# Performance work log

Measured on AMD Instinct MI355X. Metric: run time of the kernel, lower is better.

The kernel has to match this reference:

```python
import jax, jax.numpy as jnp
import numpy as np

STATIC_TH = 0.05
TRIM_RATIO = 0.2
EPS = 1e-6


def setup_inputs() -> dict:
    key = jax.random.key(0)
    k1, k2, k3 = jax.random.split(key, 3)
    B, T, H, W = 2, 32, 518, 518
    pred_disp = jax.random.uniform(k1, (B, T, H, W), jnp.float32, 0.01, 10.0)
    gt_depth = jax.random.uniform(k2, (B, T, H, W), jnp.float32, 0.1, 80.0)
    mask = jax.random.uniform(k3, (B, T, H, W)) > 0.2
    return {"pred_disp": pred_disp, "gt_depth": gt_depth, "mask": mask}


def _nanquantile_rows(vals, valid, q):
    """torch.nanquantile(dim=1, interpolation='linear') where invalid entries are NaN.
    vals: [N,Q] float, valid: [N,Q] bool. Returns [N] threshold (NaN if row empty)."""
    big = jnp.where(valid, vals, jnp.inf)          # invalid -> +inf, sorts to the end
    srt = jnp.sort(big, axis=1)                    # [N,Q]
    nv = valid.sum(axis=1)                         # valid count per row
    pos = q * jnp.maximum(nv - 1, 0).astype(vals.dtype)
    lo = jnp.floor(pos).astype(jnp.int32)
    hi = jnp.ceil(pos).astype(jnp.int32)
    frac = pos - lo.astype(vals.dtype)
    vlo = jnp.take_along_axis(srt, lo[:, None], axis=1)[:, 0]
    vhi = jnp.take_along_axis(srt, hi[:, None], axis=1)[:, 0]
    thresh = vlo * (1.0 - frac) + vhi * frac
    return jnp.where(nv > 0, thresh, jnp.nan)      # empty row -> NaN (keep-mask all False)


def reference(pred_disp, gt_depth, mask):
    B, T, H, W = pred_disp.shape
    raw = jnp.clip(pred_disp, EPS)                 # [B,T,H,W]
    gt_disp = 1.0 / jnp.clip(gt_depth, EPS)

    # per-batch least-squares scale/shift alignment on masked pixels
    raw_f = raw.reshape(B, -1)
    gt_f = gt_disp.reshape(B, -1)
    mf = mask.reshape(B, -1).astype(raw.dtype)
    count = jnp.maximum(mf.sum(axis=1, keepdims=True), 1.0)
    mean_raw = (raw_f * mf).sum(axis=1, keepdims=True) / count
    mean_gt = (gt_f * mf).sum(axis=1, keepdims=True) / count
    d_c = (raw_f - mean_raw) * mf
    g_c = (gt_f - mean_gt) * mf
    cov = (d_c * g_c).sum(axis=1, keepdims=True)
    var = jnp.maximum((d_c * d_c).sum(axis=1, keepdims=True), EPS)
    s = cov / var
    t = mean_gt - s * mean_raw
    aligned = (raw_f * s + t).reshape(B, T, H, W)

    # temporal gradient matching on static pixels
    d_diff = jnp.abs(aligned[:, 1:] - aligned[:, :-1])     # [B,T-1,H,W]
    g_diff = jnp.abs(gt_disp[:, 1:] - gt_disp[:, :-1])
    valid_pair = mask[:, 1:] & mask[:, :-1]
    depth_diff = jnp.abs(gt_depth[:, 1:] - gt_depth[:, :-1])
    static = valid_pair & (depth_diff < STATIC_TH)
    err = jnp.abs(d_diff - g_diff)

    N = B * (T - 1)
    Q = H * W
    err2 = err.reshape(N, Q)
    st2 = static.reshape(N, Q)

    # trimmed (robust) masked mean per frame pair
    thresh = _nanquantile_rows(err2, st2, 1.0 - TRIM_RATIO)   # [N]
    keep = st2 & (err2 <= thresh[:, None])
    sum_err = (err2 * keep.astype(err2.dtype)).sum(axis=1)
    cnt = jnp.maximum(keep.sum(axis=1).astype(err2.dtype), 1.0)
    loss_frame = sum_err / cnt
    return loss_frame.mean()
```

## Files before the change

kernel.cpp:

```cpp
#include <hip/hip_runtime.h>
#include <math.h>

#define HW      268324
#define HW4     67081
#define T_      32
#define B_      2
#define NPAIR   31
#define NROW    62
#define GX      263
#define CHUNKS  4
#define NBLKB   (CHUNKS*GX)
#define NFC     9
#define SLOTS   4
#define CAP     2048
#define CSTR    16
#define EPSF    1e-6f
#define STH     0.05f

typedef float fx4 __attribute__((ext_vector_type(4)));
typedef int   ix4 __attribute__((ext_vector_type(4)));


__device__ __forceinline__ float fast_rcp(float x) {
    float r = __builtin_amdgcn_rcpf(x);
    float e = fmaf(-x, r, 1.0f);
    return fmaf(r, e, r);
}

__device__ __forceinline__ fx4 nt_load4(const float* p) {
    return __builtin_nontemporal_load((const fx4*)p);
}
__device__ __forceinline__ ix4 nt_load4i(const int* p) {
    return __builtin_nontemporal_load((const ix4*)p);
}
__device__ __forceinline__ unsigned int nt_loadu(const unsigned char* p) {
    return __builtin_nontemporal_load((const unsigned int*)p);
}

template<int BYTEFMT>
__launch_bounds__(256)
__global__ void pass1_kernel(const float* __restrict__ pred,
                             const float* __restrict__ depth,
                             const void*  __restrict__ maskp,
                             double* __restrict__ partials,
                             int*    __restrict__ cnt,
                             float*  __restrict__ rbuf,
                             float*  __restrict__ gbuf,
                             float*  __restrict__ out)
{
    if (blockIdx.x == 0 && blockIdx.y == 0 && threadIdx.x == 0) out[0] = 0.0f;

    const int p4 = blockIdx.x * 256 + threadIdx.x;
    const bool active = (p4 < HW4);
    const int p4c = active ? p4 : (HW4 - 1);
    const int b = blockIdx.y >> 2;
    const int c = blockIdx.y & 3;
    const int fs = c * 8;
    const size_t base = (size_t)b * T_ * HW + (size_t)fs * HW + (size_t)p4c * 4;
    const size_t off8 = (size_t)((c == 3) ? 7 : 8) * HW;

    const float* pp = pred + base;
    const float* dd = depth + base;
    const unsigned char* m8 = (const unsigned char*)maskp + base;
    const int* m32 = (const int*)maskp + base;

    fx4 pvs[SLOTS], dvs[SLOTS];
    unsigned int mws[SLOTS];
    ix4 mis[SLOTS];

    #pragma unroll
    for (int k = 0; k < SLOTS - 1; ++k) {
        pvs[k] = nt_load4(pp + (size_t)k * HW);
        dvs[k] = nt_load4(dd + (size_t)k * HW);
        if (BYTEFMT) mws[k] = nt_loadu(m8 + (size_t)k * HW);
        else         mis[k] = nt_load4i(m32 + (size_t)k * HW);
    }

    int scn = 0;
    float f_r = 0.f, f_g = 0.f, f_rg = 0.f, f_rr = 0.f;
    float pcr[4], pcg[4], pcd[4];
    unsigned int pmb = 0u;

    #pragma unroll
    for (int k = 0; k < NFC; ++k) {
        const int kp = k + SLOTS - 1;
        if (kp < NFC) {
            const size_t off = (kp < 8) ? (size_t)kp * HW : off8;
            const int s2 = kp % SLOTS;
            pvs[s2] = nt_load4(pp + off);
            dvs[s2] = nt_load4(dd + off);
            if (BYTEFMT) mws[s2] = nt_loadu(m8 + off);
            else         mis[s2] = nt_load4i(m32 + off);
        }
        const int s = k % SLOTS;
        unsigned int mb;
        if (BYTEFMT) {
            const unsigned int w = mws[s];
            mb = ((w & 0x000000FFu) ? 1u : 0u) | ((w & 0x0000FF00u) ? 2u : 0u)
               | ((w & 0x00FF0000u) ? 4u : 0u) | ((w & 0xFF000000u) ? 8u : 0u);
        } else {
            const ix4 mi = mis[s];
            mb = (mi.x ? 1u : 0u) | (mi.y ? 2u : 0u) | (mi.z ? 4u : 0u) | (mi.w ? 8u : 0u);
        }
        if (!active) mb = 0u;

        const float px[4] = {pvs[s].x, pvs[s].y, pvs[s].z, pvs[s].w};
        const float dx[4] = {dvs[s].x, dvs[s].y, dvs[s].z, dvs[s].w};
        float cr[4], cg[4], cd[4];
        #pragma unroll
        for (int j = 0; j < 4; ++j) {
            cr[j] = fmaxf(px[j], EPSF);
            cd[j] = dx[j];
            cg[j] = fast_rcp(fmaxf(dx[j], EPSF));
        }

        if (k <= 7) {
            #pragma unroll
            for (int j = 0; j < 4; ++j) {
                const bool m = (mb >> j) & 1u;
                const float rm = m ? cr[j] : 0.0f;
                const float gm = m ? cg[j] : 0.0f;
                scn += m ? 1 : 0;
                f_r += rm; f_g += gm;
                f_rg = fmaf(rm, gm, f_rg);
                f_rr = fmaf(rm, rm, f_rr);
            }
        }

        if (k >= 1 && (k <= 7 || c < 3)) {
            const int row = b * NPAIR + fs + k - 1;
            #pragma unroll
            for (int j = 0; j < 4; ++j) {
                if (((mb >> j) & (pmb >> j) & 1u) && fabsf(cd[j] - pcd[j]) < STH) {
                    const int pos = atomicAdd(&cnt[row * CSTR], 1);
                    if (pos < CAP) {
                        rbuf[row * CAP + pos] = fabsf(cr[j] - pcr[j]);
                        gbuf[row * CAP + pos] = fabsf(cg[j] - pcg[j]);
                    }
                }
            }
        }

        #pragma unroll
        for (int j = 0; j < 4; ++j) { pcr[j] = cr[j]; pcg[j] = cg[j]; pcd[j] = cd[j]; }
        pmb = mb;
    }

    double v1 = (double)f_r, v2 = (double)f_g, v3 = (double)f_rg, v4 = (double)f_rr;
    int vc = scn;
    #pragma unroll
    for (int o = 32; o > 0; o >>= 1) {
        v1 += __shfl_down(v1, o); v2 += __shfl_down(v2, o);
        v3 += __shfl_down(v3, o); v4 += __shfl_down(v4, o);
        vc += __shfl_down(vc, o);
    }
    __shared__ double red[4][4];
    __shared__ int redc[4];
    const int wid = threadIdx.x >> 6, lane = threadIdx.x & 63;
    if (lane == 0) { red[wid][0]=v1; red[wid][1]=v2; red[wid][2]=v3; red[wid][3]=v4; redc[wid]=vc; }
    __syncthreads();
    if (threadIdx.x == 0) {
        double* p = partials + (size_t)(blockIdx.y * GX + blockIdx.x) * 5;
        p[0] = (double)(redc[0] + redc[1] + redc[2] + redc[3]);
        p[1] = red[0][0]+red[1][0]+red[2][0]+red[3][0];
        p[2] = red[0][1]+red[1][1]+red[2][1]+red[3][1];
        p[3] = red[0][2]+red[1][2]+red[2][2]+red[3][2];
        p[4] = red[0][3]+red[1][3]+red[2][3]+red[3][3];
    }
}

__launch_bounds__(256)
__global__ void rowquant_kernel(const double* __restrict__ partials,
                                const int* __restrict__ cnt,
                                const float* __restrict__ rbuf,
                                const float* __restrict__ gbuf,
                                float* __restrict__ out)
{
    __shared__ float arr[CAP];
    __shared__ double rs[4][5];
    __shared__ float s_sa;
    __shared__ int   s_P;
    const int row = blockIdx.x;
    const int bb  = row / NPAIR;
    const int wid = threadIdx.x >> 6, lane = threadIdx.x & 63;

    const double* p = partials + (size_t)bb * NBLKB * 5;
    double v[5] = {0, 0, 0, 0, 0};
    for (int i = threadIdx.x; i < NBLKB; i += 256) {
        #pragma unroll
        for (int j = 0; j < 5; ++j) v[j] += p[i * 5 + j];
    }
    #pragma unroll
    for (int o = 32; o > 0; o >>= 1) {
        #pragma unroll
        for (int j = 0; j < 5; ++j) v[j] += __shfl_down(v[j], o);
    }
    if (lane == 0) {
        #pragma unroll
        for (int j = 0; j < 5; ++j) rs[wid][j] = v[j];
    }
    __syncthreads();

    int n = cnt[row * CSTR]; if (n > CAP) n = CAP;
    if (threadIdx.x == 0) {
        const double c0  = rs[0][0]+rs[1][0]+rs[2][0]+rs[3][0];
        const double sr  = rs[0][1]+rs[1][1]+rs[2][1]+rs[3][1];
        const double sg  = rs[0][2]+rs[1][2]+rs[2][2]+rs[3][2];
        const double srg = rs[0][3]+rs[1][3]+rs[2][3]+rs[3][3];
        const double srr = rs[0][4]+rs[1][4]+rs[2][4]+rs[3][4];
        const double count = fmax(c0, 1.0);
        const double mr = sr / count, mg = sg / count;
        const double cov = srg - mr * sg - mg * sr + c0 * mr * mg;
        double       var = srr - 2.0 * mr * sr + c0 * mr * mr;
        var = fmax(var, 1e-6);
        s_sa = (float)fabs(cov / var);
        int P = 64; while (P < n) P <<= 1;
        s_P = P;
    }
    __syncthreads();
    const float sa = s_sa;
    const int   P  = s_P;

    for (int i = threadIdx.x; i < P; i += 256) {
        float e = INFINITY;
        if (i < n) e = fabsf(sa * rbuf[row * CAP + i] - gbuf[row * CAP + i]);
        arr[i] = e;
    }
    __syncthreads();

    for (int k = 2; k <= P; k <<= 1) {
        for (int j = k >> 1; j > 0; j >>= 1) {
            for (int i = threadIdx.x; i < P; i += 256) {
                const int ij = i ^ j;
                if (ij > i) {
                    const float a = arr[i], bv = arr[ij];
                    const bool up = ((i & k) == 0);
                    if ((a > bv) == up) { arr[i] = bv; arr[ij] = a; }
                }
            }
            __syncthreads();
        }
    }

    __shared__ float sthresh;
    if (threadIdx.x == 0) {
        if (n > 0) {
            const float pos  = 0.8f * (float)(n - 1);
            const int   lo   = (int)floorf(pos);
            const int   hi   = (int)ceilf(pos);
            const float frac = pos - (float)lo;
            sthresh = arr[lo] * (1.0f - frac) + arr[hi] * frac;
        } else {
            sthresh = -1.0f;
        }
    }
    __syncthreads();
    const float th = sthresh;

    double lsum = 0.0; int lcnt = 0;
    for (int i = threadIdx.x; i < n; i += 256) {
        const float e = arr[i];
        if (e <= th) { lsum += (double)e; lcnt++; }
    }
    #pragma unroll
    for (int o = 32; o > 0; o >>= 1) { lsum += __shfl_down(lsum, o); lcnt += __shfl_down(lcnt, o); }
    __shared__ double rr2[4]; __shared__ int rc2[4];
    if (lane == 0) { rr2[wid] = lsum; rc2[wid] = lcnt; }
    __syncthreads();
    if (threadIdx.x == 0) {
        const double tot = rr2[0] + rr2[1] + rr2[2] + rr2[3];
        const int    tc  = rc2[0] + rc2[1] + rc2[2] + rc2[3];
        const double loss_row = tot / (double)(tc > 0 ? tc : 1);
        atomicAdd(out, (float)(loss_row * (1.0 / (double)NROW)));
    }
}

extern "C" void kernel_launch(void* const* d_in, const int* in_sizes, int n_in,
                              void* d_out, int out_size, void* d_ws, size_t ws_size,
                              hipStream_t stream) {
    const float* pred  = (const float*)d_in[0];
    const float* depth = (const float*)d_in[1];
    const void*  mask  = d_in[2];
    float* out = (float*)d_out;

    char* ws = (char*)d_ws;
    int*    cnt        = (int*)(ws + 64);
    double* partials   = (double*)(ws + 8192);
    float*  rbuf       = (float*)(ws + 180224);
    float*  gbuf       = (float*)(ws + 688128);

    const int byteFmt = (in_sizes[2] != in_sizes[0]) ? 1 : 0;

    hipMemsetAsync(ws + 64, 0, 3968, stream);

    dim3 g1(GX, B_ * CHUNKS);
    if (byteFmt)
        pass1_kernel<1><<<g1, 256, 0, stream>>>(pred, depth, mask, partials, cnt, rbuf, gbuf, out);
    else
        pass1_kernel<0><<<g1, 256, 0, stream>>>(pred, depth, mask, partials, cnt, rbuf, gbuf, out);
    rowquant_kernel<<<NROW, 256, 0, stream>>>(partials, cnt, rbuf, gbuf, out);
}
```

Baseline: 203.3 us.

## Split frames into eight chunks of four and load all frames upfront

Result: no change. 205.7 us (+1.2%).

```diff
diff --git a/kernel.cpp b/kernel.cpp
--- a/kernel.cpp
+++ b/kernel.cpp
@@ -8,10 +8,9 @@
 #define NPAIR   31
 #define NROW    62
 #define GX      263
-#define CHUNKS  4
+#define CHUNKS  8
 #define NBLKB   (CHUNKS*GX)
-#define NFC     9
-#define SLOTS   4
+#define NFC     5
 #define CAP     2048
 #define CSTR    16
 #define EPSF    1e-6f
@@ -53,27 +52,27 @@
     const int p4 = blockIdx.x * 256 + threadIdx.x;
     const bool active = (p4 < HW4);
     const int p4c = active ? p4 : (HW4 - 1);
-    const int b = blockIdx.y >> 2;
-    const int c = blockIdx.y & 3;
-    const int fs = c * 8;
+    const int b = blockIdx.y >> 3;
+    const int c = blockIdx.y & 7;
+    const int fs = c * 4;
     const size_t base = (size_t)b * T_ * HW + (size_t)fs * HW + (size_t)p4c * 4;
-    const size_t off8 = (size_t)((c == 3) ? 7 : 8) * HW;
 
     const float* pp = pred + base;
     const float* dd = depth + base;
     const unsigned char* m8 = (const unsigned char*)maskp + base;
     const int* m32 = (const int*)maskp + base;
 
-    fx4 pvs[SLOTS], dvs[SLOTS];
-    unsigned int mws[SLOTS];
-    ix4 mis[SLOTS];
-
-    #pragma unroll
-    for (int k = 0; k < SLOTS - 1; ++k) {
-        pvs[k] = nt_load4(pp + (size_t)k * HW);
-        dvs[k] = nt_load4(dd + (size_t)k * HW);
-        if (BYTEFMT) mws[k] = nt_loadu(m8 + (size_t)k * HW);
-        else         mis[k] = nt_load4i(m32 + (size_t)k * HW);
+    const size_t off4 = (size_t)((c == 7) ? 3 : 4) * HW;
+    fx4 pvs[NFC], dvs[NFC];
+    unsigned int mws[NFC];
+    ix4 mis[NFC];
+    #pragma unroll
+    for (int k = 0; k < NFC; ++k) {
+        const size_t off = (k < 4) ? (size_t)k * HW : off4;
+        pvs[k] = nt_load4(pp + off);
+        dvs[k] = nt_load4(dd + off);
+        if (BYTEFMT) mws[k] = nt_loadu(m8 + off);
+        else         mis[k] = nt_load4i(m32 + off);
     }
 
     int scn = 0;
@@ -83,29 +82,19 @@
 
     #pragma unroll
     for (int k = 0; k < NFC; ++k) {
-        const int kp = k + SLOTS - 1;
-        if (kp < NFC) {
-            const size_t off = (kp < 8) ? (size_t)kp * HW : off8;
-            const int s2 = kp % SLOTS;
-            pvs[s2] = nt_load4(pp + off);
-            dvs[s2] = nt_load4(dd + off);
-            if (BYTEFMT) mws[s2] = nt_loadu(m8 + off);
-            else         mis[s2] = nt_load4i(m32 + off);
-        }
-        const int s = k % SLOTS;
         unsigned int mb;
         if (BYTEFMT) {
-            const unsigned int w = mws[s];
+            const unsigned int w = mws[k];
             mb = ((w & 0x000000FFu) ? 1u : 0u) | ((w & 0x0000FF00u) ? 2u : 0u)
                | ((w & 0x00FF0000u) ? 4u : 0u) | ((w & 0xFF000000u) ? 8u : 0u);
         } else {
-            const ix4 mi = mis[s];
+            const ix4 mi = mis[k];
             mb = (mi.x ? 1u : 0u) | (mi.y ? 2u : 0u) | (mi.z ? 4u : 0u) | (mi.w ? 8u : 0u);
         }
         if (!active) mb = 0u;
 
-        const float px[4] = {pvs[s].x, pvs[s].y, pvs[s].z, pvs[s].w};
-        const float dx[4] = {dvs[s].x, dvs[s].y, dvs[s].z, dvs[s].w};
+        const float px[4] = {pvs[k].x, pvs[k].y, pvs[k].z, pvs[k].w};
+        const float dx[4] = {dvs[k].x, dvs[k].y, dvs[k].z, dvs[k].w};
         float cr[4], cg[4], cd[4];
         #pragma unroll
         for (int j = 0; j < 4; ++j) {
@@ -114,7 +103,7 @@
             cg[j] = fast_rcp(fmaxf(dx[j], EPSF));
         }
 
-        if (k <= 7) {
+        if (k <= 3) {
             #pragma unroll
             for (int j = 0; j < 4; ++j) {
                 const bool m = (mb >> j) & 1u;
@@ -127,7 +116,7 @@
             }
         }
 
-        if (k >= 1 && (k <= 7 || c < 3)) {
+        if (k >= 1 && (k <= 3 || c < 7)) {
             const int row = b * NPAIR + fs + k - 1;
             #pragma unroll
             for (int j = 0; j < 4; ++j) {
```
